# Kernel tuning notes

Hardware: AMD Instinct MI355X
Metric: run time of the kernel (lower is better)

Reference implementation:

```python
import jax, jax.numpy as jnp
import numpy as np

MARGIN = 1.0


def setup_inputs() -> dict:
    key = jax.random.key(0)
    k1, k2 = jax.random.split(key)
    inputs = jax.random.normal(k1, (512, 256), dtype=jnp.float32)
    targets = jax.random.randint(k2, (512,), 0, 64)
    return {"inputs": inputs, "targets": targets}


def reference(inputs, targets):
    n = inputs.shape[0]
    # pairwise euclidean distance matrix [n, n]
    sq = jnp.sum(inputs * inputs, axis=1)
    dist = sq[:, None] + sq[None, :] - 2.0 * (inputs @ inputs.T)
    dist = jnp.sqrt(jnp.clip(dist, 1e-16))

    # triplet margins: ap_dist[i,j] - an_dist[i,k] + margin -> [n, n, n]
    triplet = dist[:, :, None] - dist[:, None, :] + MARGIN

    # mask: i != j, i != k, j != k, labels[i]==labels[j], labels[i]!=labels[k]
    not_eye = ~jnp.eye(n, dtype=bool)
    dist_idx = not_eye[:, :, None] & not_eye[:, None, :] & not_eye[None, :, :]
    teq = targets[:, None] == targets[None, :]  # symmetric [n, n]
    valid = teq[:, :, None] & (~teq[:, None, :])
    mask = (valid & dist_idx).astype(triplet.dtype)

    triplet = jnp.maximum(mask * triplet, 0.0)
    num_triplets = jnp.sum((triplet > 1e-16).astype(triplet.dtype))
    return jnp.sum(triplet) / (num_triplets + 1e-16)
```

## Files before the change

kernel.cpp:

```cpp
#include <hip/hip_runtime.h>

constexpr int N = 512;
constexpr int D = 256;
#define MARGIN 1.0f

__device__ __forceinline__ float dpp_add16(float v) {
  v += __int_as_float(__builtin_amdgcn_update_dpp(
      0, __float_as_int(v), 0x118, 0xF, 0xF, true));
  v += __int_as_float(__builtin_amdgcn_update_dpp(
      0, __float_as_int(v), 0x114, 0xF, 0xF, true));
  v += __int_as_float(__builtin_amdgcn_update_dpp(
      0, __float_as_int(v), 0x112, 0xF, 0xF, true));
  v += __int_as_float(__builtin_amdgcn_update_dpp(
      0, __float_as_int(v), 0x111, 0xF, 0xF, true));
  return v;
}

#define ACC(S, A, B)                                                   \
  { float ex = A.x - B.x, ey = A.y - B.y, ez = A.z - B.z,              \
          ew = A.w - B.w;                                              \
    S += ex * ex + ey * ey + ez * ez + ew * ew; }

__global__ __launch_bounds__(1024, 4) void triplet_fused(
    const float* __restrict__ x, const int* __restrict__ tgt,
    float* __restrict__ part) {
  __shared__ __align__(16) float m0[N], m1[N];
  __shared__ float cl0[N], cl1[N];
  __shared__ int ts[N];
  __shared__ int nv0, nv1;
  __shared__ float wred[32];

  const int b = blockIdx.x;
  const int i0 = 2 * b, i1 = 2 * b + 1;
  const int tid = threadIdx.x;
  const int wave = tid >> 6, lane = tid & 63;
  const int sub = lane & 15, rg = lane >> 4;

  if (tid == 0) { nv0 = 0; nv1 = 0; }
  if (tid < N) ts[tid] = tgt[tid];

  const float4* xa = (const float4*)(x + (size_t)i0 * D);
  const float4* xc = (const float4*)(x + (size_t)i1 * D);
  float4 a0 = xa[sub], a1 = xa[16 + sub], a2 = xa[32 + sub], a3 = xa[48 + sub];
  float4 c0 = xc[sub], c1 = xc[16 + sub], c2 = xc[32 + sub], c3 = xc[48 + sub];
  __syncthreads();
  const int t0 = ts[i0], t1 = ts[i1];

  const int rot = (b * 171) & (N - 1);
  const int rbase = wave * 32 + rg;

  int r = (rbase + rot) & (N - 1);
  const float4* xr = (const float4*)(x + (size_t)r * D);
  float4 b0 = xr[sub], b1 = xr[16 + sub], b2 = xr[32 + sub], b3 = xr[48 + sub];

  #pragma unroll 2
  for (int it = 0; it < 8; ++it) {
    const int rn = (rbase + (((it + 1) & 7) << 2) + rot) & (N - 1);
    const float4* xn = (const float4*)(x + (size_t)rn * D);
    float4 p0 = xn[sub], p1 = xn[16 + sub], p2 = xn[32 + sub], p3 = xn[48 + sub];

    float sa = 0.f, sb = 0.f;
    ACC(sa, a0, b0); ACC(sa, a1, b1); ACC(sa, a2, b2); ACC(sa, a3, b3);
    ACC(sb, c0, b0); ACC(sb, c1, b1); ACC(sb, c2, b2); ACC(sb, c3, b3);
    sa = dpp_add16(sa);
    sb = dpp_add16(sb);
    if (sub == 15) {
      const int tj = ts[r];
      float da = sqrtf(fmaxf(sa, 1e-16f));
      float db = sqrtf(fmaxf(sb, 1e-16f));
      m0[r] = (tj != t0) ? da : __builtin_inff();
      m1[r] = (tj != t1) ? db : __builtin_inff();
      if (tj == t0 && r != i0) { int s = atomicAdd(&nv0, 1); cl0[s] = da + MARGIN; }
      if (tj == t1 && r != i1) { int s = atomicAdd(&nv1, 1); cl1[s] = db + MARGIN; }
    }
    b0 = p0; b1 = p1; b2 = p2; b3 = p3;
    r = rn;
  }
  __syncthreads();

  float sum = 0.f, cnt = 0.f;
  const int e = tid & 511, half = tid >> 9;
  const float mk0 = m0[e], mk1 = m1[e];
  const int n0 = nv0, n1 = nv1;
  for (int v = half; v < n0; v += 2) {
    float a = cl0[v] - mk0;
    sum += fmaxf(a, 0.f);
    cnt += (a > 1e-16f ? 1.f : 0.f);
  }
  for (int v = half; v < n1; v += 2) {
    float a = cl1[v] - mk1;
    sum += fmaxf(a, 0.f);
    cnt += (a > 1e-16f ? 1.f : 0.f);
  }

  #pragma unroll
  for (int off = 32; off > 0; off >>= 1) {
    sum += __shfl_down(sum, off);
    cnt += __shfl_down(cnt, off);
  }
  if (lane == 0) { wred[wave] = sum; wred[16 + wave] = cnt; }
  __syncthreads();
  if (tid == 0) {
    float s = 0.f, c = 0.f;
    #pragma unroll
    for (int w = 0; w < 16; ++w) { s += wred[w]; c += wred[16 + w]; }
    part[2 * b] = s;
    part[2 * b + 1] = c;
  }
}

__global__ __launch_bounds__(256) void triplet_finalize(
    const float* __restrict__ part, float* __restrict__ out) {
  __shared__ float wred[8];
  const int tid = threadIdx.x;
  float s = part[2 * tid], c = part[2 * tid + 1];
  #pragma unroll
  for (int off = 32; off > 0; off >>= 1) {
    s += __shfl_down(s, off);
    c += __shfl_down(c, off);
  }
  int wave = tid >> 6, lane = tid & 63;
  if (lane == 0) { wred[wave] = s; wred[4 + wave] = c; }
  __syncthreads();
  if (tid == 0) {
    float ts = wred[0] + wred[1] + wred[2] + wred[3];
    float tc = wred[4] + wred[5] + wred[6] + wred[7];
    out[0] = ts / (tc + 1e-16f);
  }
}

extern "C" void kernel_launch(void* const* d_in, const int* in_sizes, int n_in,
                              void* d_out, int out_size, void* d_ws, size_t ws_size,
                              hipStream_t stream) {
  const float* x = (const float*)d_in[0];
  const int* tgt = (const int*)d_in[1];
  float* out = (float*)d_out;
  float* part = (float*)d_ws;

  triplet_fused<<<N / 2, 1024, 0, stream>>>(x, tgt, part);
  triplet_finalize<<<1, 256, 0, stream>>>(part, out);
}
```

Measured before the change: 64.87 us.

## Fuse finalize into main kernel via atomic ticket and deepen row prefetch

Removes the second finalize launch. Each block atomically adds its partial sum and count to global accumulators, and the last block to take a ticket computes the final ratio and resets the state. The row-streaming loop also prefetches two rows ahead instead of one, to hide more global load latency. The trade-offs are float atomic ordering nondeterminism, reliance on device-global state that must reset correctly between calls, and higher register use.

```diff
diff --git a/kernel.cpp b/kernel.cpp
--- a/kernel.cpp
+++ b/kernel.cpp
@@ -3,6 +3,10 @@
 constexpr int N = 512;
 constexpr int D = 256;
 #define MARGIN 1.0f
+
+__device__ float g_sum = 0.f;
+__device__ float g_cnt = 0.f;
+__device__ int g_ticket = 0;
 
 __device__ __forceinline__ float dpp_add16(float v) {
   v += __int_as_float(__builtin_amdgcn_update_dpp(
@@ -23,7 +27,7 @@
 
 __global__ __launch_bounds__(1024, 4) void triplet_fused(
     const float* __restrict__ x, const int* __restrict__ tgt,
-    float* __restrict__ part) {
+    float* __restrict__ out) {
   __shared__ __align__(16) float m0[N], m1[N];
   __shared__ float cl0[N], cl1[N];
   __shared__ int ts[N];
@@ -49,15 +53,21 @@
   const int rot = (b * 171) & (N - 1);
   const int rbase = wave * 32 + rg;
 
-  int r = (rbase + rot) & (N - 1);
-  const float4* xr = (const float4*)(x + (size_t)r * D);
-  float4 b0 = xr[sub], b1 = xr[16 + sub], b2 = xr[32 + sub], b3 = xr[48 + sub];
+  int rc = (rbase + rot) & (N - 1);
+  int rn = (rbase + 4 + rot) & (N - 1);
+  const float4* xr0 = (const float4*)(x + (size_t)rc * D);
+  float4 b0 = xr0[sub], b1 = xr0[16 + sub], b2 = xr0[32 + sub],
+         b3 = xr0[48 + sub];
+  const float4* xr1 = (const float4*)(x + (size_t)rn * D);
+  float4 n0 = xr1[sub], n1 = xr1[16 + sub], n2 = xr1[32 + sub],
+         n3 = xr1[48 + sub];
 
   #pragma unroll 2
   for (int it = 0; it < 8; ++it) {
-    const int rn = (rbase + (((it + 1) & 7) << 2) + rot) & (N - 1);
-    const float4* xn = (const float4*)(x + (size_t)rn * D);
-    float4 p0 = xn[sub], p1 = xn[16 + sub], p2 = xn[32 + sub], p3 = xn[48 + sub];
+    const int rp = (rbase + (((it + 2) & 7) << 2) + rot) & (N - 1);
+    const float4* xp = (const float4*)(x + (size_t)rp * D);
+    float4 p0 = xp[sub], p1 = xp[16 + sub], p2 = xp[32 + sub],
+           p3 = xp[48 + sub];
 
     float sa = 0.f, sb = 0.f;
     ACC(sa, a0, b0); ACC(sa, a1, b1); ACC(sa, a2, b2); ACC(sa, a3, b3);
@@ -65,29 +75,30 @@
     sa = dpp_add16(sa);
     sb = dpp_add16(sb);
     if (sub == 15) {
-      const int tj = ts[r];
+      const int tj = ts[rc];
       float da = sqrtf(fmaxf(sa, 1e-16f));
       float db = sqrtf(fmaxf(sb, 1e-16f));
-      m0[r] = (tj != t0) ? da : __builtin_inff();
-      m1[r] = (tj != t1) ? db : __builtin_inff();
-      if (tj == t0 && r != i0) { int s = atomicAdd(&nv0, 1); cl0[s] = da + MARGIN; }
-      if (tj == t1 && r != i1) { int s = atomicAdd(&nv1, 1); cl1[s] = db + MARGIN; }
+      m0[rc] = (tj != t0) ? da : __builtin_inff();
+      m1[rc] = (tj != t1) ? db : __builtin_inff();
+      if (tj == t0 && rc != i0) { int s = atomicAdd(&nv0, 1); cl0[s] = da + MARGIN; }
+      if (tj == t1 && rc != i1) { int s = atomicAdd(&nv1, 1); cl1[s] = db + MARGIN; }
     }
-    b0 = p0; b1 = p1; b2 = p2; b3 = p3;
-    r = rn;
+    b0 = n0; b1 = n1; b2 = n2; b3 = n3;
+    n0 = p0; n1 = p1; n2 = p2; n3 = p3;
+    rc = rn; rn = rp;
   }
   __syncthreads();
 
   float sum = 0.f, cnt = 0.f;
   const int e = tid & 511, half = tid >> 9;
   const float mk0 = m0[e], mk1 = m1[e];
-  const int n0 = nv0, n1 = nv1;
-  for (int v = half; v < n0; v += 2) {
+  const int nn0 = nv0, nn1 = nv1;
+  for (int v = half; v < nn0; v += 2) {
     float a = cl0[v] - mk0;
     sum += fmaxf(a, 0.f);
     cnt += (a > 1e-16f ? 1.f : 0.f);
   }
-  for (int v = half; v < n1; v += 2) {
+  for (int v = half; v < nn1; v += 2) {
     float a = cl1[v] - mk1;
     sum += fmaxf(a, 0.f);
     cnt += (a > 1e-16f ? 1.f : 0.f);
@@ -100,32 +111,23 @@
   }
   if (lane == 0) { wred[wave] = sum; wred[16 + wave] = cnt; }
   __syncthreads();
+
   if (tid == 0) {
     float s = 0.f, c = 0.f;
     #pragma unroll
     for (int w = 0; w < 16; ++w) { s += wred[w]; c += wred[16 + w]; }
-    part[2 * b] = s;
-    part[2 * b + 1] = c;
-  }
-}
-
-__global__ __launch_bounds__(256) void triplet_finalize(
-    const float* __restrict__ part, float* __restrict__ out) {
-  __shared__ float wred[8];
-  const int tid = threadIdx.x;
-  float s = part[2 * tid], c = part[2 * tid + 1];
-  #pragma unroll
-  for (int off = 32; off > 0; off >>= 1) {
-    s += __shfl_down(s, off);
-    c += __shfl_down(c, off);
-  }
-  int wave = tid >> 6, lane = tid & 63;
-  if (lane == 0) { wred[wave] = s; wred[4 + wave] = c; }
-  __syncthreads();
-  if (tid == 0) {
-    float ts = wred[0] + wred[1] + wred[2] + wred[3];
-    float tc = wred[4] + wred[5] + wred[6] + wred[7];
-    out[0] = ts / (tc + 1e-16f);
+    atomicAdd(&g_sum, s);
+    atomicAdd(&g_cnt, c);
+    asm volatile("s_waitcnt vmcnt(0)" ::: "memory");
+    const int old = atomicAdd(&g_ticket, 1);
+    if (old == N / 2 - 1) {
+      const float tsum = atomicAdd(&g_sum, 0.f);
+      const float tcnt = atomicAdd(&g_cnt, 0.f);
+      out[0] = tsum / (tcnt + 1e-16f);
+      atomicExch(&g_sum, 0.f);
+      atomicExch(&g_cnt, 0.f);
+      atomicExch(&g_ticket, 0);
+    }
   }
 }
 
@@ -135,8 +137,7 @@
   const float* x = (const float*)d_in[0];
   const int* tgt = (const int*)d_in[1];
   float* out = (float*)d_out;
-  float* part = (float*)d_ws;
+  (void)d_ws; (void)ws_size;
 
-  triplet_fused<<<N / 2, 1024, 0, stream>>>(x, tgt, part);
-  triplet_finalize<<<1, 256, 0, stream>>>(part, out);
+  triplet_fused<<<N / 2, 1024, 0, stream>>>(x, tgt, out);
 }
```

Result: slower. 73.86 us (+13.9%).
